# Kernel tuning notes

Measured on AMD Instinct MI355X. Metric: run time of the kernel, lower is better.

Reference implementation:

```python
import jax, jax.numpy as jnp
import numpy as np

L = 2        # gnn_layers
D = 256      # hidden_dim
E = 1024     # emb_dim
NCLS = 7
NEG = 1e30


def lstm_cell(x, h, c, Wih, Whh, bih, bhh):
    # torch.nn.LSTMCell math; gate order i, f, g, o
    g = x @ Wih.T + bih + h @ Whh.T + bhh
    i, f, gg, o = jnp.split(g, 4, axis=-1)
    c2 = jax.nn.sigmoid(f) * c + jax.nn.sigmoid(i) * jnp.tanh(gg)
    return jax.nn.sigmoid(o) * jnp.tanh(c2), c2


def dag_layer(Hl, adj_f, W1, W2, Wr, Wc_ih, Wc_hh, bc_ih, bc_hh, Wp_ih, Wp_hh, bp_ih, bp_hh):
    # Hl: (B,N,D). Sequential DAG recurrence with dot-product attention over growing prefix.
    B, N, Dh = Hl.shape
    zeros = jnp.zeros((B, Dh), Hl.dtype)
    h0 = Hl[:, 0]
    C0, _ = lstm_cell(h0, zeros, zeros, Wc_ih, Wc_hh, bc_ih, bc_hh)
    P0, _ = lstm_cell(zeros, h0, h0, Wp_ih, Wp_hh, bp_ih, bp_hh)
    Ht0 = C0 + P0
    # carry pre-projected keys/values incrementally to avoid O(N^2 D^2) work
    K2 = jnp.zeros((B, N, Dh), Hl.dtype).at[:, 0].set(Ht0 @ W2.T)
    Vr = jnp.zeros((B, N, Dh), Hl.dtype).at[:, 0].set(Ht0 @ Wr.T)
    H1 = jnp.zeros((B, N, Dh), Hl.dtype).at[:, 0].set(Ht0)
    pos = jnp.arange(N)

    def step(carry, i):
        K2, Vr, H1 = carry
        Q = jax.lax.dynamic_index_in_dim(Hl, i, axis=1, keepdims=False)      # (B,D)
        adj_i = jax.lax.dynamic_index_in_dim(adj_f, i, axis=1, keepdims=False)  # (B,N)
        q = Q @ W1.T
        logits = jnp.einsum('bd,bnd->bn', q, K2) - (1.0 - adj_i) * NEG  # mask_logic
        logits = jnp.where(pos[None, :] < i, logits, -NEG)              # only prefix :i
        w = jax.nn.softmax(logits, axis=-1)
        M = jnp.einsum('bn,bnd->bd', w, Vr)
        C, _ = lstm_cell(Q, M, M, Wc_ih, Wc_hh, bc_ih, bc_hh)
        P, _ = lstm_cell(M, Q, Q, Wp_ih, Wp_hh, bp_ih, bp_hh)
        Ht = C + P
        K2 = K2.at[:, i].set(Ht @ W2.T)
        Vr = Vr.at[:, i].set(Ht @ Wr.T)
        H1 = H1.at[:, i].set(Ht)
        return (K2, Vr, H1), None

    (K2, Vr, H1), _ = jax.lax.scan(step, (K2, Vr, H1), jnp.arange(1, N))
    return H1


def setup_inputs() -> dict:
    key = jax.random.key(0)
    ks = iter(jax.random.split(key, 40))
    B, N = 16, 128
    s = lambda *sh: jax.random.normal(next(ks), sh, jnp.float32) * 0.02
    in_dim = D * (L + 1) + E
    return dict(
        features=jax.random.normal(next(ks), (B, N, E), jnp.float32),
        adj=jnp.ones((B, N, N), jnp.int32),
        s_mask=jnp.zeros((B, N, N), jnp.int32),
        s_mask_onehot=jnp.zeros((B, N, N, 2), jnp.int32),
        lengths=jnp.ones((B,), jnp.int32) * N,
        fc1_W=s(D, E), fc1_b=jnp.zeros((D,), jnp.float32),
        W1=s(L, D, D), W2=s(L, D, D), Wr=s(L, D, D),
        Wc_ih=s(L, 4 * D, D), Wc_hh=s(L, 4 * D, D),
        bc_ih=jnp.zeros((L, 4 * D), jnp.float32), bc_hh=jnp.zeros((L, 4 * D), jnp.float32),
        Wp_ih=s(L, 4 * D, D), Wp_hh=s(L, 4 * D, D),
        bp_ih=jnp.zeros((L, 4 * D), jnp.float32), bp_hh=jnp.zeros((L, 4 * D), jnp.float32),
        m0_W=s(D, in_dim), m0_b=jnp.zeros((D,), jnp.float32),
        m1_W=s(D, D), m1_b=jnp.zeros((D,), jnp.float32),
        m2_W=s(NCLS, D), m2_b=jnp.zeros((NCLS,), jnp.float32),
    )


def reference(features, adj, s_mask, s_mask_onehot, lengths,
              fc1_W, fc1_b, W1, W2, Wr,
              Wc_ih, Wc_hh, bc_ih, bc_hh,
              Wp_ih, Wp_hh, bp_ih, bp_hh,
              m0_W, m0_b, m1_W, m1_b, m2_W, m2_b):
    # s_mask / s_mask_onehot unused for attn_type='dotprod', no_rel_attn=True
    # lengths unused for nodal_att_type=None (attentive_node_features is identity)
    adj_f = adj.astype(features.dtype)
    H0 = jax.nn.relu(features @ fc1_W.T + fc1_b)
    Hs = [H0]
    for l in range(L):
        Hs.append(dag_layer(Hs[l], adj_f,
                            W1[l], W2[l], Wr[l],
                            Wc_ih[l], Wc_hh[l], bc_ih[l], bc_hh[l],
                            Wp_ih[l], Wp_hh[l], bp_ih[l], bp_hh[l]))
    Hcat = jnp.concatenate(Hs + [features], axis=2)  # (B,N,D*(L+1)+E)
    h = jax.nn.relu(Hcat @ m0_W.T + m0_b)
    h = jax.nn.relu(h @ m1_W.T + m1_b)  # mlp_layers-1 extra layer; dropout p=0 -> identity
    return h @ m2_W.T + m2_b            # (B,N,num_class)
```

## Files before the change

### kernel.cpp

```cpp
#include <hip/hip_runtime.h>
#include <hip/hip_fp16.h>
#include <math.h>

#define B_ 16
#define N_ 128
#define D_ 256
#define E_ 1024
#define GD4 1024
#define SENT 0xFFC0DEADu

typedef _Float16 h2 __attribute__((ext_vector_type(2)));
typedef _Float16 f16x8 __attribute__((ext_vector_type(8)));
typedef float f32x4 __attribute__((ext_vector_type(4)));

__device__ __forceinline__ float dot2w(unsigned w, h2 hv, float acc) {
#if __has_builtin(__builtin_amdgcn_fdot2)
  return __builtin_amdgcn_fdot2(__builtin_bit_cast(h2, w), hv, acc, false);
#else
  union { unsigned u; _Float16 e[2]; } c; c.u = w;
  return acc + (float)c.e[0]*(float)hv.x + (float)c.e[1]*(float)hv.y;
#endif
}
__device__ __forceinline__ float dot2h(h2 a, h2 b, float acc) {
#if __has_builtin(__builtin_amdgcn_fdot2)
  return __builtin_amdgcn_fdot2(a, b, acc, false);
#else
  return acc + (float)a.x*(float)b.x + (float)a.y*(float)b.y;
#endif
}

template<bool BIAS, bool RELU>
__global__ __launch_bounds__(256) void gemm_k(const float* __restrict__ X,
    const float* __restrict__ W, const float* __restrict__ bias,
    float* __restrict__ C, int M, int N, int K)
{
  __shared__ float Xs[32][68];
  __shared__ float Ws[32][68];
  const int tid = threadIdx.x;
  const int m0 = blockIdx.x * 64, n0 = blockIdx.y * 64;
  const int tm = tid >> 4, tn = tid & 15;
  float acc[4][4] = {};
  for (int k0 = 0; k0 < K; k0 += 32) {
    for (int e = tid; e < 2048; e += 256) {
      int mm = e >> 5, kk = e & 31;
      Xs[kk][mm] = X[(m0+mm)*K + k0+kk];
    }
    for (int e = tid; e < 2048; e += 256) {
      int nn = e >> 5, kk = e & 31;
      Ws[kk][nn] = (n0+nn < N) ? W[(n0+nn)*K + k0+kk] : 0.f;
    }
    __syncthreads();
    for (int kk = 0; kk < 32; kk++) {
      float4 a = *(const float4*)&Xs[kk][tm*4];
      float4 b = *(const float4*)&Ws[kk][tn*4];
      acc[0][0] += a.x*b.x; acc[0][1] += a.x*b.y; acc[0][2] += a.x*b.z; acc[0][3] += a.x*b.w;
      acc[1][0] += a.y*b.x; acc[1][1] += a.y*b.y; acc[1][2] += a.y*b.z; acc[1][3] += a.y*b.w;
      acc[2][0] += a.z*b.x; acc[2][1] += a.z*b.y; acc[2][2] += a.z*b.z; acc[2][3] += a.z*b.w;
      acc[3][0] += a.w*b.x; acc[3][1] += a.w*b.y; acc[3][2] += a.w*b.z; acc[3][3] += a.w*b.w;
    }
    __syncthreads();
  }
  for (int i2 = 0; i2 < 4; i2++) {
    int row = m0 + tm*4 + i2;
    for (int j2 = 0; j2 < 4; j2++) {
      int col = n0 + tn*4 + j2;
      if (col < N) {
        float v = acc[i2][j2];
        if (BIAS) v += bias[col];
        if (RELU) v = fmaxf(v, 0.f);
        C[row*N + col] = v;
      }
    }
  }
}

__device__ __forceinline__ void mf_stage(const float* __restrict__ src,
    int ldsrc, _Float16 (*dst)[264], int tid)
{
  for (int e = tid; e < 8192; e += 256) {
    int row = e >> 7, cp = e & 127;
    float2 v = *(const float2*)&src[(size_t)row*ldsrc + 2*cp];
    h2 t; t.x = (_Float16)v.x; t.y = (_Float16)v.y;
    *(h2*)&dst[row][2*cp] = t;
  }
}

__device__ __forceinline__ void mf_compute(_Float16 (*Xh)[264],
    _Float16 (*Wh)[264], f32x4 acc[2][2], int l, int wr, int wc)
{
  #pragma unroll
  for (int kc = 0; kc < 256; kc += 32) {
    f16x8 a0 = *(const f16x8*)&Xh[wr*32 +      (l & 15)][kc + (l >> 4)*8];
    f16x8 a1 = *(const f16x8*)&Xh[wr*32 + 16 + (l & 15)][kc + (l >> 4)*8];
    f16x8 b0 = *(const f16x8*)&Wh[wc*32 +      (l & 15)][kc + (l >> 4)*8];
    f16x8 b1 = *(const f16x8*)&Wh[wc*32 + 16 + (l & 15)][kc + (l >> 4)*8];
    acc[0][0] = __builtin_amdgcn_mfma_f32_16x16x32_f16(a0, b0, acc[0][0], 0, 0, 0);
    acc[0][1] = __builtin_amdgcn_mfma_f32_16x16x32_f16(a0, b1, acc[0][1], 0, 0, 0);
    acc[1][0] = __builtin_amdgcn_mfma_f32_16x16x32_f16(a1, b0, acc[1][0], 0, 0, 0);
    acc[1][1] = __builtin_amdgcn_mfma_f32_16x16x32_f16(a1, b1, acc[1][1], 0, 0, 0);
  }
}

template<bool BIAS, bool RELU>
__global__ __launch_bounds__(256) void mfgemm_k(const float* __restrict__ X,
    const float* __restrict__ W, const float* __restrict__ bias,
    float* __restrict__ C, int M, int N, int K)
{
  __shared__ _Float16 Xh[64][264];
  __shared__ _Float16 Wh[64][264];
  const int tid = threadIdx.x;
  const int m0 = blockIdx.x * 64, n0 = blockIdx.y * 64;
  const int l = tid & 63, w = tid >> 6;
  const int wr = w >> 1, wc = w & 1;
  f32x4 acc[2][2];
  #pragma unroll
  for (int rt = 0; rt < 2; ++rt)
    #pragma unroll
    for (int ct = 0; ct < 2; ++ct) acc[rt][ct] = 0.f;
  for (int k0 = 0; k0 < K; k0 += 256) {
    mf_stage(X + (size_t)m0*K + k0, K, Xh, tid);
    mf_stage(W + (size_t)n0*K + k0, K, Wh, tid);
    __syncthreads();
    mf_compute(Xh, Wh, acc, l, wr, wc);
    __syncthreads();
  }
  #pragma unroll
  for (int rt = 0; rt < 2; ++rt)
    #pragma unroll
    for (int ct = 0; ct < 2; ++ct)
      #pragma unroll
      for (int j = 0; j < 4; ++j) {
        int row = m0 + wr*32 + rt*16 + (l >> 4)*4 + j;
        int col = n0 + wc*32 + ct*16 + (l & 15);
        float v = acc[rt][ct][j];
        if (BIAS) v += bias[col];
        if (RELU) v = fmaxf(v, 0.f);
        C[(size_t)row*N + col] = v;
      }
}

__global__ __launch_bounds__(256) void prologue_mf_k(const float* __restrict__ X,
    const float* __restrict__ Wc, const float* __restrict__ Wp,
    const float* __restrict__ Am, const float* __restrict__ bcc,
    const float* __restrict__ bpc, float* __restrict__ GQC,
    float* __restrict__ GQP, float* __restrict__ VM)
{
  __shared__ _Float16 Xh[64][264];
  __shared__ _Float16 Wh[64][264];
  const int tid = threadIdx.x;
  const int m0 = blockIdx.x * 64;
  const int nt = blockIdx.y;
  const float* W; const float* bias; float* C; int n0; int NC;
  if (nt < 16)      { W = Wc; bias = bcc;     C = GQC; n0 = nt*64;      NC = 1024; }
  else if (nt < 32) { W = Wp; bias = bpc;     C = GQP; n0 = (nt-16)*64; NC = 1024; }
  else              { W = Am; bias = nullptr; C = VM;  n0 = (nt-32)*64; NC = 256;  }
  const int l = tid & 63, w = tid >> 6;
  const int wr = w >> 1, wc = w & 1;
  f32x4 acc[2][2];
  #pragma unroll
  for (int rt = 0; rt < 2; ++rt)
    #pragma unroll
    for (int ct = 0; ct < 2; ++ct) acc[rt][ct] = 0.f;
  mf_stage(X + (size_t)m0*256, 256, Xh, tid);
  mf_stage(W + (size_t)n0*256, 256, Wh, tid);
  __syncthreads();
  mf_compute(Xh, Wh, acc, l, wr, wc);
  __syncthreads();
  #pragma unroll
  for (int rt = 0; rt < 2; ++rt)
    #pragma unroll
    for (int ct = 0; ct < 2; ++ct)
      #pragma unroll
      for (int j = 0; j < 4; ++j) {
        int row = m0 + wr*32 + rt*16 + (l >> 4)*4 + j;
        int col = n0 + wc*32 + ct*16 + (l & 15);
        float v = acc[rt][ct][j];
        if (bias) v += bias[col];
        C[(size_t)row*NC + col] = v;
      }
}

__global__ __launch_bounds__(256) void m0fused_mf_k(const float* __restrict__ H0,
    const float* __restrict__ H1, const float* __restrict__ H2,
    const float* __restrict__ feat, const float* __restrict__ W,
    const float* __restrict__ bias, float* __restrict__ C)
{
  __shared__ _Float16 Xh[64][264];
  __shared__ _Float16 Wh[64][264];
  const int tid = threadIdx.x;
  const int m0 = blockIdx.x * 64, n0 = blockIdx.y * 64;
  const int l = tid & 63, w = tid >> 6;
  const int wr = w >> 1, wc = w & 1;
  f32x4 acc[2][2];
  #pragma unroll
  for (int rt = 0; rt < 2; ++rt)
    #pragma unroll
    for (int ct = 0; ct < 2; ++ct) acc[rt][ct] = 0.f;
  for (int k0 = 0; k0 < 1792; k0 += 256) {
    const float* src; int lds_; int coff;
    if (k0 == 0)        { src = H0;   lds_ = 256;  coff = 0; }
    else if (k0 == 256) { src = H1;   lds_ = 256;  coff = 0; }
    else if (k0 == 512) { src = H2;   lds_ = 256;  coff = 0; }
    else                { src = feat; lds_ = 1024; coff = k0 - 768; }
    mf_stage(src + (size_t)m0*lds_ + coff, lds_, Xh, tid);
    mf_stage(W + (size_t)n0*1792 + k0, 1792, Wh, tid);
    __syncthreads();
    mf_compute(Xh, Wh, acc, l, wr, wc);
    __syncthreads();
  }
  #pragma unroll
  for (int rt = 0; rt < 2; ++rt)
    #pragma unroll
    for (int ct = 0; ct < 2; ++ct)
      #pragma unroll
      for (int j = 0; j < 4; ++j) {
        int row = m0 + wr*32 + rt*16 + (l >> 4)*4 + j;
        int col = n0 + wc*32 + ct*16 + (l & 15);
        C[(size_t)row*256 + col] = fmaxf(acc[rt][ct][j] + bias[col], 0.f);
      }
}

__global__ __launch_bounds__(256) void prepamat_k(const float* __restrict__ W2,
    const float* __restrict__ W1, float* __restrict__ AM)
{
  __shared__ float Xs[32][68];
  __shared__ float Ws[32][68];
  const int tid = threadIdx.x;
  const int m0 = blockIdx.x * 64, n0 = blockIdx.y * 64;
  const float* X = W2 + blockIdx.z * 65536;
  const float* W = W1 + blockIdx.z * 65536;
  float* C = AM + blockIdx.z * 65536;
  const int tm = tid >> 4, tn = tid & 15;
  float acc[4][4] = {};
  for (int k0 = 0; k0 < 256; k0 += 32) {
    for (int e = tid; e < 2048; e += 256) {
      int kk = e >> 6, mm = e & 63;
      Xs[kk][mm] = X[(k0+kk)*256 + m0+mm];
    }
    for (int e = tid; e < 2048; e += 256) {
      int kk = e >> 6, nn = e & 63;
      Ws[kk][nn] = W[(k0+kk)*256 + n0+nn];
    }
    __syncthreads();
    for (int kk = 0; kk < 32; kk++) {
      float4 a = *(const float4*)&Xs[kk][tm*4];
      float4 b = *(const float4*)&Ws[kk][tn*4];
      acc[0][0] += a.x*b.x; acc[0][1] += a.x*b.y; acc[0][2] += a.x*b.z; acc[0][3] += a.x*b.w;
      acc[1][0] += a.y*b.x; acc[1][1] += a.y*b.y; acc[1][2] += a.y*b.z; acc[1][3] += a.y*b.w;
      acc[2][0] += a.z*b.x; acc[2][1] += a.z*b.y; acc[2][2] += a.z*b.z; acc[2][3] += a.z*b.w;
      acc[3][0] += a.w*b.x; acc[3][1] += a.w*b.y; acc[3][2] += a.w*b.z; acc[3][3] += a.w*b.w;
    }
    __syncthreads();
  }
  for (int i2 = 0; i2 < 4; i2++)
    for (int j2 = 0; j2 < 4; j2++)
      C[(m0 + tm*4 + i2)*256 + n0 + tn*4 + j2] = acc[i2][j2];
}

__global__ __launch_bounds__(256) void prepnn_k(const float* __restrict__ Wch,
    const float* __restrict__ Wpi, const float* __restrict__ Wr,
    float* __restrict__ OUT)
{
  __shared__ float Xs[32][68];
  __shared__ float Ws[32][68];
  const int tid = threadIdx.x;
  const int m0 = blockIdx.x * 64, n0 = blockIdx.y * 64;
  const int l = blockIdx.z;
  const float* X = (m0 < 1024) ? (Wch + l*262144 + m0*256)
                               : (Wpi + l*262144 + (m0-1024)*256);
  const float* W = Wr + l*65536;
  float* C = OUT + l*524288;
  const int tm = tid >> 4, tn = tid & 15;
  float acc[4][4] = {};
  for (int k0 = 0; k0 < 256; k0 += 32) {
    for (int e = tid; e < 2048; e += 256) {
      int mm = e >> 5, kk = e & 31;
      Xs[kk][mm] = X[mm*256 + k0+kk];
    }
    for (int e = tid; e < 2048; e += 256) {
      int kk = e >> 6, nn = e & 63;
      Ws[kk][nn] = W[(k0+kk)*256 + n0+nn];
    }
    __syncthreads();
    for (int kk = 0; kk < 32; kk++) {
      float4 a = *(const float4*)&Xs[kk][tm*4];
      float4 b = *(const float4*)&Ws[kk][tn*4];
      acc[0][0] += a.x*b.x; acc[0][1] += a.x*b.y; acc[0][2] += a.x*b.z; acc[0][3] += a.x*b.w;
      acc[1][0] += a.y*b.x; acc[1][1] += a.y*b.y; acc[1][2] += a.y*b.z; acc[1][3] += a.y*b.w;
      acc[2][0] += a.z*b.x; acc[2][1] += a.z*b.y; acc[2][2] += a.z*b.z; acc[2][3] += a.z*b.w;
      acc[3][0] += a.w*b.x; acc[3][1] += a.w*b.y; acc[3][2] += a.w*b.z; acc[3][3] += a.w*b.w;
    }
    __syncthreads();
  }
  for (int i2 = 0; i2 < 4; i2++)
    for (int j2 = 0; j2 < 4; j2++)
      C[(m0 + tm*4 + i2)*256 + n0 + tn*4 + j2] = acc[i2][j2];
}

__global__ void bias_sum_k(const float* __restrict__ bci, const float* __restrict__ bch,
                           const float* __restrict__ bpi, const float* __restrict__ bph,
                           float* __restrict__ bcC, float* __restrict__ bpC)
{
  int i = blockIdx.x*256 + threadIdx.x;
  if (i < 2048) { bcC[i] = bci[i] + bch[i]; bpC[i] = bpi[i] + bph[i]; }
}

__global__ void pack_k(const float* __restrict__ wchpi, const float* __restrict__ wr,
                       _Float16* __restrict__ out)
{
  int idx = blockIdx.x*256 + threadIdx.x;
  int l  = idx / 589824; int rem = idx % 589824;
  int sl = rem / 36864;  int rem2 = rem % 36864;
  int cq = rem2 / 1152;  int rem3 = rem2 % 1152;
  int r  = rem3 >> 3;    int e = rem3 & 7;
  int c  = cq*8 + e;
  int g  = r >> 4, dl = r & 15;
  int d  = sl*16 + dl;
  float v;
  if (g < 8) v = wchpi[l*524288 + (g*256 + d)*256 + c];
  else       v = wr[l*65536 + d*256 + c];
  out[idx] = (_Float16)v;
}

__global__ void fill_k(unsigned* __restrict__ a, unsigned* __restrict__ b)
{
  int i = blockIdx.x*256 + threadIdx.x;
  if (i < 524288) {
    __hip_atomic_store(a + i, SENT, __ATOMIC_RELAXED, __HIP_MEMORY_SCOPE_AGENT);
    __hip_atomic_store(b + i, SENT, __ATOMIC_RELAXED, __HIP_MEMORY_SCOPE_AGENT);
  }
}

__device__ __forceinline__ float sigf(float x) { return 1.f / (1.f + __expf(-x)); }
__device__ __forceinline__ float tanhfast(float x) {
  float xc = fminf(fmaxf(x, -15.f), 15.f);
  float e = __expf(-2.f * xc);
  return (1.f - e) / (1.f + e);
}

__global__ __launch_bounds__(512, 2) void scan_k(
    const float* __restrict__ Hl,
    const float* __restrict__ Vm,
    const float* __restrict__ gqC,
    const float* __restrict__ gqP,
    const _Float16* __restrict__ WTp,
    const int*   __restrict__ adj,
    float* __restrict__ Hout)
{
  __shared__ uint4 wl4[4608];
  __shared__ float G[128*144];
  __shared__ __align__(8) _Float16 h2s[256];
  __shared__ float v_s[256];
  __shared__ __align__(8) _Float16 v2s[256];
  __shared__ float psum[128];
  __shared__ float aw[128];
  __shared__ int   adj_s[2][128];
  __shared__ float gqc_l[2][64], gqp_l[2][64];
  __shared__ float ql[2][16];
  __shared__ float Gg[144];
  __shared__ float red[2];
  __shared__ float sinv;

  const int tid = threadIdx.x;
  const int b   = blockIdx.x >> 4;
  const int sl  = blockIdx.x & 15;

  { const uint4* src = (const uint4*)WTp + (size_t)sl*4608;
    for (int e = tid; e < 4608; e += 512) wl4[e] = src[e]; }

  const int rr_ = tid >> 2;
  const int rj  = tid & 3;

#define PREF(ip_, bf_) do {                                                    \
    int ip = (ip_); int bf = (bf_);                                            \
    for (int u = tid - 288; u < 528; u += 224) {                               \
      if (u < 256) { float v = Vm[(b*N_ + ip)*D_ + u]; v_s[u] = v;             \
                     v2s[u] = (_Float16)v; }                                   \
      else if (u < 384) adj_s[bf][u-256] = adj[(b*N_ + ip)*N_ + (u-256)];      \
      else if (u < 448) gqc_l[bf][u-384] = gqC[(b*N_+ip)*GD4 + ((u-384)>>4)*D_ + sl*16 + ((u-384)&15)]; \
      else if (u < 512) gqp_l[bf][u-448] = gqP[(b*N_+ip)*GD4 + ((u-448)>>4)*D_ + sl*16 + ((u-448)&15)]; \
      else ql[bf][u-512] = Hl[(b*N_+ip)*D_ + sl*16 + (u-512)];                 \
    }                                                                          \
  } while (0)

  if (tid >= 288) PREF(0, 0);
  __syncthreads();

  for (int i = 0; i < N_; ++i) {
    const int cur = i & 1;
    if (i > 0) {
      if (rr_ + 1 < i) {
        const float4* hp = (const float4*)(Hout + ((size_t)(b*N_ + rr_))*D_) + rj;
        const float4* vv = (const float4*)v_s + rj;
        float4 areg[16];
        #pragma unroll
        for (int c4 = 0; c4 < 16; ++c4) areg[c4] = hp[c4*4];
        float acc = 0.f;
        #pragma unroll
        for (int c4 = 0; c4 < 16; ++c4) {
          float4 a = areg[c4], w = vv[c4*4];
          acc += a.x*w.x + a.y*w.y + a.z*w.z + a.w*w.w;
        }
        acc += __shfl_xor(acc, 1, 64);
        acc += __shfl_xor(acc, 2, 64);
        if (rj == 0) psum[rr_] = acc;
      }
      if (tid >= 448) {
        const unsigned* wp = (const unsigned*)Hout
                           + ((size_t)(b*N_ + (i-1)))*D_ + ((tid-448)&15)*16 + 15;
        while (__hip_atomic_load(wp, __ATOMIC_RELAXED, __HIP_MEMORY_SCOPE_AGENT) == SENT)
          __builtin_amdgcn_s_sleep(1);
        int lane = tid - 448;
        float4 hv = *((const float4*)(Hout + ((size_t)(b*N_ + (i-1)))*D_) + lane);
        h2* hd = (h2*)h2s + lane*2;
        h2 t0; t0.x = (_Float16)hv.x; t0.y = (_Float16)hv.y;
        h2 t1; t1.x = (_Float16)hv.z; t1.y = (_Float16)hv.w;
        hd[0] = t0; hd[1] = t1;
      }
      __syncthreads();
      asm volatile("" ::: "memory");

      if (tid < 288) {
        int r = tid >> 1, hf = tid & 1;
        float acc2 = 0.f;
        #pragma unroll 4
        for (int it = 0; it < 16; ++it) {
          int cq = hf*16 + it;
          uint4 w4 = wl4[cq*144 + r];
          const h2* hh = (const h2*)h2s + cq*4;
          acc2 = dot2w(w4.x, hh[0], acc2);
          acc2 = dot2w(w4.y, hh[1], acc2);
          acc2 = dot2w(w4.z, hh[2], acc2);
          acc2 = dot2w(w4.w, hh[3], acc2);
        }
        acc2 += __shfl_xor(acc2, 1, 64);
        if (!hf) G[(i-1)*144 + r] = acc2;
      }
      if (rr_ == i-1) {
        const h2* hh = (const h2*)h2s + rj*32;
        const h2* vv = (const h2*)v2s + rj*32;
        float acc = 0.f;
        #pragma unroll 8
        for (int q = 0; q < 32; ++q) acc = dot2h(hh[q], vv[q], acc);
        acc += __shfl_xor(acc, 1, 64);
        acc += __shfl_xor(acc, 2, 64);
        if (rj == 0) psum[i-1] = acc;
      }
      if (tid >= 320 && tid < 448) {
        int k = tid - 320;
        float e = (k + 1 < i && adj_s[cur][k] != 0) ? __expf(psum[k]) : 0.f;
        aw[k] = e;
        float sv = e;
        #pragma unroll
        for (int off = 32; off >= 1; off >>= 1) sv += __shfl_xor(sv, off, 64);
        if ((k & 63) == 0) red[k >> 6] = sv;
      }
      __syncthreads();

      if (tid < 288) {
        int r = tid >> 1, kh = tid & 1;
        float e1 = (adj_s[cur][i-1] != 0) ? __expf(psum[i-1]) : 0.f;
        float g = kh ? e1 * G[(i-1)*144 + r] : 0.f;
        int m = i - 1;
        int k0 = kh ? (m >> 1) : 0, k1 = kh ? m : (m >> 1);
        for (int k = k0; k < k1; ++k) g += aw[k] * G[k*144 + r];
        g += __shfl_xor(g, 1, 64);
        if (!kh) Gg[r] = g;
        if (tid == 0) sinv = 1.f / (red[0] + red[1] + e1);
      } else {
        PREF((i < 127) ? i+1 : 127, (i+1) & 1);
      }
      __syncthreads();
    } else {
      if (tid >= 288) PREF(1, 1);
      __syncthreads();
    }

    if (tid < 32) {
      int dl = tid >> 1, cell = tid & 1;
      float inv = (i > 0) ? sinv : 0.f;
      float r0 = 0.f, r1 = 0.f, r2 = 0.f, r3 = 0.f, Mv = 0.f;
      if (i > 0) {
        r0 = Gg[(cell*4+0)*16 + dl] * inv;
        r1 = Gg[(cell*4+1)*16 + dl] * inv;
        r2 = Gg[(cell*4+2)*16 + dl] * inv;
        r3 = Gg[(cell*4+3)*16 + dl] * inv;
        Mv = Gg[128 + dl] * inv;
      }
      float Qv = ql[cur][dl];
      const float* gq = cell ? &gqp_l[cur][0] : &gqc_l[cur][0];
      float xi = cell ? Qv : Mv;
      float gi_ = r0 + gq[ 0 + dl];
      float gf_ = r1 + gq[16 + dl];
      float gg_ = r2 + gq[32 + dl];
      float go_ = r3 + gq[48 + dl];
      float c2  = sigf(gf_)*xi + sigf(gi_)*tanhfast(gg_);
      float ov  = sigf(go_)*tanhfast(c2);
      float htv = ov + __shfl_xor(ov, 1, 64);
      if (!cell) {
        __hip_atomic_store(&Hout[((size_t)(b*N_ + i))*D_ + sl*16 + dl], htv,
                           __ATOMIC_RELAXED, __HIP_MEMORY_SCOPE_AGENT);
      }
    }
  }
#undef PREF
}

extern "C" void kernel_launch(void* const* d_in, const int* in_sizes, int n_in,
                              void* d_out, int out_size, void* d_ws, size_t ws_size,
                              hipStream_t stream)
{
  const float* features = (const float*)d_in[0];
  const int*   adj      = (const int*)  d_in[1];
  const float* fc1_W    = (const float*)d_in[5];
  const float* fc1_b    = (const float*)d_in[6];
  const float* W1       = (const float*)d_in[7];
  const float* W2       = (const float*)d_in[8];
  const float* Wr       = (const float*)d_in[9];
  const float* Wc_ih    = (const float*)d_in[10];
  const float* Wc_hh    = (const float*)d_in[11];
  const float* bc_ih    = (const float*)d_in[12];
  const float* bc_hh    = (const float*)d_in[13];
  const float* Wp_ih    = (const float*)d_in[14];
  const float* Wp_hh    = (const float*)d_in[15];
  const float* bp_ih    = (const float*)d_in[16];
  const float* bp_hh    = (const float*)d_in[17];
  const float* m0_W     = (const float*)d_in[18];
  const float* m0_b     = (const float*)d_in[19];
  const float* m1_W     = (const float*)d_in[20];
  const float* m1_b     = (const float*)d_in[21];
  const float* m2_W     = (const float*)d_in[22];
  const float* m2_b     = (const float*)d_in[23];

  float* ws = (float*)d_ws;
  _Float16* WTP = (_Float16*)ws;
  float* AMAT   = ws + 589824;
  float* BCC    = ws + 720896;
  float* BPC    = ws + 722944;
  float* WCHPI  = ws + 724992;
  float* H0     = ws + 1773568;
  float* H1     = ws + 2297856;
  float* H2     = ws + 2822144;
  float* VMAT   = ws + 3346432;
  float* GQC    = ws + 3870720;
  float* GQP    = ws + 5967872;
  float* HB1    = ws + 8065024;
  float* HB2    = ws + 8589312;

  fill_k<<<2048, 256, 0, stream>>>((unsigned*)H1, (unsigned*)H2);
  bias_sum_k<<<8, 256, 0, stream>>>(bc_ih, bc_hh, bp_ih, bp_hh, BCC, BPC);
  prepamat_k<<<dim3(4,4,2), 256, 0, stream>>>(W2, W1, AMAT);
  prepnn_k<<<dim3(32,4,2), 256, 0, stream>>>(Wc_hh, Wp_ih, Wr, WCHPI);
  pack_k<<<4608, 256, 0, stream>>>(WCHPI, Wr, WTP);

  mfgemm_k<true,true><<<dim3(32,4), 256, 0, stream>>>(features, fc1_W, fc1_b, H0, 2048, 256, 1024);

  prologue_mf_k<<<dim3(32,36), 256, 0, stream>>>(H0, Wc_ih, Wp_hh, AMAT,
                                                 BCC, BPC, GQC, GQP, VMAT);
  scan_k<<<256, 512, 0, stream>>>(H0, VMAT, GQC, GQP, WTP, adj, H1);

  prologue_mf_k<<<dim3(32,36), 256, 0, stream>>>(H1, Wc_ih + 262144, Wp_hh + 262144,
                                                 AMAT + 65536, BCC + 1024, BPC + 1024,
                                                 GQC, GQP, VMAT);
  scan_k<<<256, 512, 0, stream>>>(H1, VMAT, GQC, GQP, WTP + 589824, adj, H2);

  m0fused_mf_k<<<dim3(32,4), 256, 0, stream>>>(H0, H1, H2, features, m0_W, m0_b, HB1);
  mfgemm_k<true,true><<<dim3(32,4), 256, 0, stream>>>(HB1, m1_W, m1_b, HB2, 2048, 256, 256);
  gemm_k<true,false><<<dim3(32,1), 256, 0, stream>>>(HB2, m2_W, m2_b, (float*)d_out, 2048, 7, 256);
}
```

Before: 1.785 ms.

## Fuse weight packing into prep GEMM, drop bias kernel, shrink sentinel fill

Measured after the change: 1.824 ms. 2.2% more time.

```diff
diff --git a/kernel.cpp b/kernel.cpp
--- a/kernel.cpp
+++ b/kernel.cpp
@@ -141,8 +141,9 @@
 
 __global__ __launch_bounds__(256) void prologue_mf_k(const float* __restrict__ X,
     const float* __restrict__ Wc, const float* __restrict__ Wp,
-    const float* __restrict__ Am, const float* __restrict__ bcc,
-    const float* __restrict__ bpc, float* __restrict__ GQC,
+    const float* __restrict__ Am, const float* __restrict__ bci,
+    const float* __restrict__ bch, const float* __restrict__ bpi,
+    const float* __restrict__ bph, float* __restrict__ GQC,
     float* __restrict__ GQP, float* __restrict__ VM)
 {
   __shared__ _Float16 Xh[64][264];
@@ -150,10 +151,10 @@
   const int tid = threadIdx.x;
   const int m0 = blockIdx.x * 64;
   const int nt = blockIdx.y;
-  const float* W; const float* bias; float* C; int n0; int NC;
-  if (nt < 16)      { W = Wc; bias = bcc;     C = GQC; n0 = nt*64;      NC = 1024; }
-  else if (nt < 32) { W = Wp; bias = bpc;     C = GQP; n0 = (nt-16)*64; NC = 1024; }
-  else              { W = Am; bias = nullptr; C = VM;  n0 = (nt-32)*64; NC = 256;  }
+  const float* W; const float* b0; const float* b1; float* C; int n0; int NC;
+  if (nt < 16)      { W = Wc; b0 = bci; b1 = bch;  C = GQC; n0 = nt*64;      NC = 1024; }
+  else if (nt < 32) { W = Wp; b0 = bpi; b1 = bph;  C = GQP; n0 = (nt-16)*64; NC = 1024; }
+  else              { W = Am; b0 = nullptr; b1 = nullptr; C = VM; n0 = (nt-32)*64; NC = 256; }
   const int l = tid & 63, w = tid >> 6;
   const int wr = w >> 1, wc = w & 1;
   f32x4 acc[2][2];
@@ -175,7 +176,7 @@
         int row = m0 + wr*32 + rt*16 + (l >> 4)*4 + j;
         int col = n0 + wc*32 + ct*16 + (l & 15);
         float v = acc[rt][ct][j];
-        if (bias) v += bias[col];
+        if (b0) v += b0[col] + b1[col];
         C[(size_t)row*NC + col] = v;
       }
 }
@@ -259,7 +260,7 @@
 
 __global__ __launch_bounds__(256) void prepnn_k(const float* __restrict__ Wch,
     const float* __restrict__ Wpi, const float* __restrict__ Wr,
-    float* __restrict__ OUT)
+    _Float16* __restrict__ WTP)
 {
   __shared__ float Xs[32][68];
   __shared__ float Ws[32][68];
@@ -269,7 +270,6 @@
   const float* X = (m0 < 1024) ? (Wch + l*262144 + m0*256)
                                : (Wpi + l*262144 + (m0-1024)*256);
   const float* W = Wr + l*65536;
-  float* C = OUT + l*524288;
   const int tm = tid >> 4, tn = tid & 15;
   float acc[4][4] = {};
   for (int k0 = 0; k0 < 256; k0 += 32) {
@@ -292,42 +292,35 @@
     }
     __syncthreads();
   }
-  for (int i2 = 0; i2 < 4; i2++)
-    for (int j2 = 0; j2 < 4; j2++)
-      C[(m0 + tm*4 + i2)*256 + n0 + tn*4 + j2] = acc[i2][j2];
-}
-
-__global__ void bias_sum_k(const float* __restrict__ bci, const float* __restrict__ bch,
-                           const float* __restrict__ bpi, const float* __restrict__ bph,
-                           float* __restrict__ bcC, float* __restrict__ bpC)
+  for (int i2 = 0; i2 < 4; i2++) {
+    int row = m0 + tm*4 + i2;
+    int g = (row < 1024) ? (row >> 8) : (4 + ((row - 1024) >> 8));
+    int d = row & 255;
+    int slp = d >> 4, dl = d & 15, r = g*16 + dl;
+    size_t base = (size_t)l*589824 + (size_t)slp*36864 + r*8;
+    for (int j2 = 0; j2 < 4; j2++) {
+      int c = n0 + tn*4 + j2;
+      WTP[base + (size_t)(c >> 3)*1152 + (c & 7)] = (_Float16)acc[i2][j2];
+    }
+  }
+}
+
+__global__ void wrpack_k(const float* __restrict__ wr, _Float16* __restrict__ WTP)
+{
+  int idx = blockIdx.x*256 + threadIdx.x;
+  int l = idx >> 16; int rem = idx & 65535;
+  int d = rem >> 8; int c = rem & 255;
+  int slp = d >> 4, dl = d & 15;
+  WTP[(size_t)l*589824 + (size_t)slp*36864 + (size_t)(c >> 3)*1152
+      + (128 + dl)*8 + (c & 7)] = (_Float16)wr[l*65536 + d*256 + c];
+}
+
+__global__ void fill_k(unsigned* __restrict__ a, unsigned* __restrict__ b)
 {
   int i = blockIdx.x*256 + threadIdx.x;
-  if (i < 2048) { bcC[i] = bci[i] + bch[i]; bpC[i] = bpi[i] + bph[i]; }
-}
-
-__global__ void pack_k(const float* __restrict__ wchpi, const float* __restrict__ wr,
-                       _Float16* __restrict__ out)
-{
-  int idx = blockIdx.x*256 + threadIdx.x;
-  int l  = idx / 589824; int rem = idx % 589824;
-  int sl = rem / 36864;  int rem2 = rem % 36864;
-  int cq = rem2 / 1152;  int rem3 = rem2 % 1152;
-  int r  = rem3 >> 3;    int e = rem3 & 7;
-  int c  = cq*8 + e;
-  int g  = r >> 4, dl = r & 15;
-  int d  = sl*16 + dl;
-  float v;
-  if (g < 8) v = wchpi[l*524288 + (g*256 + d)*256 + c];
-  else       v = wr[l*65536 + d*256 + c];
-  out[idx] = (_Float16)v;
-}
-
-__global__ void fill_k(unsigned* __restrict__ a, unsigned* __restrict__ b)
-{
-  int i = blockIdx.x*256 + threadIdx.x;
-  if (i < 524288) {
-    __hip_atomic_store(a + i, SENT, __ATOMIC_RELAXED, __HIP_MEMORY_SCOPE_AGENT);
-    __hip_atomic_store(b + i, SENT, __ATOMIC_RELAXED, __HIP_MEMORY_SCOPE_AGENT);
+  if (i < 32768) {
+    __hip_atomic_store(a + i*16 + 15, SENT, __ATOMIC_RELAXED, __HIP_MEMORY_SCOPE_AGENT);
+    __hip_atomic_store(b + i*16 + 15, SENT, __ATOMIC_RELAXED, __HIP_MEMORY_SCOPE_AGENT);
   }
 }
 
@@ -406,13 +399,16 @@
         if (rj == 0) psum[rr_] = acc;
       }
       if (tid >= 448) {
+        int L = tid - 448;
         const unsigned* wp = (const unsigned*)Hout
-                           + ((size_t)(b*N_ + (i-1)))*D_ + ((tid-448)&15)*16 + 15;
-        while (__hip_atomic_load(wp, __ATOMIC_RELAXED, __HIP_MEMORY_SCOPE_AGENT) == SENT)
-          __builtin_amdgcn_s_sleep(1);
-        int lane = tid - 448;
-        float4 hv = *((const float4*)(Hout + ((size_t)(b*N_ + (i-1)))*D_) + lane);
-        h2* hd = (h2*)h2s + lane*2;
+                           + ((size_t)(b*N_ + (i-1)))*D_ + (L & 15)*16 + 15;
+        unsigned v;
+        do {
+          v = (L < 16) ? __hip_atomic_load(wp, __ATOMIC_RELAXED, __HIP_MEMORY_SCOPE_AGENT)
+                       : 0u;
+        } while (__ballot((L < 16) && (v == SENT)));
+        float4 hv = *((const float4*)(Hout + ((size_t)(b*N_ + (i-1)))*D_) + L);
+        h2* hd = (h2*)h2s + L*2;
         h2 t0; t0.x = (_Float16)hv.x; t0.y = (_Float16)hv.y;
         h2 t1; t1.x = (_Float16)hv.z; t1.y = (_Float16)hv.w;
         hd[0] = t0; hd[1] = t1;
@@ -535,32 +531,31 @@
   float* ws = (float*)d_ws;
   _Float16* WTP = (_Float16*)ws;
   float* AMAT   = ws + 589824;
-  float* BCC    = ws + 720896;
-  float* BPC    = ws + 722944;
-  float* WCHPI  = ws + 724992;
-  float* H0     = ws + 1773568;
-  float* H1     = ws + 2297856;
-  float* H2     = ws + 2822144;
-  float* VMAT   = ws + 3346432;
-  float* GQC    = ws + 3870720;
-  float* GQP    = ws + 5967872;
-  float* HB1    = ws + 8065024;
-  float* HB2    = ws + 8589312;
-
-  fill_k<<<2048, 256, 0, stream>>>((unsigned*)H1, (unsigned*)H2);
-  bias_sum_k<<<8, 256, 0, stream>>>(bc_ih, bc_hh, bp_ih, bp_hh, BCC, BPC);
+  float* H0     = ws + 720896;
+  float* H1     = ws + 1245184;
+  float* H2     = ws + 1769472;
+  float* VMAT   = ws + 2293760;
+  float* GQC    = ws + 2818048;
+  float* GQP    = ws + 4915200;
+  float* HB1    = ws + 7012352;
+  float* HB2    = ws + 7536640;
+
+  fill_k<<<128, 256, 0, stream>>>((unsigned*)H1, (unsigned*)H2);
   prepamat_k<<<dim3(4,4,2), 256, 0, stream>>>(W2, W1, AMAT);
-  prepnn_k<<<dim3(32,4,2), 256, 0, stream>>>(Wc_hh, Wp_ih, Wr, WCHPI);
-  pack_k<<<4608, 256, 0, stream>>>(WCHPI, Wr, WTP);
+  prepnn_k<<<dim3(32,4,2), 256, 0, stream>>>(Wc_hh, Wp_ih, Wr, WTP);
+  wrpack_k<<<512, 256, 0, stream>>>(Wr, WTP);
 
   mfgemm_k<true,true><<<dim3(32,4), 256, 0, stream>>>(features, fc1_W, fc1_b, H0, 2048, 256, 1024);
 
   prologue_mf_k<<<dim3(32,36), 256, 0, stream>>>(H0, Wc_ih, Wp_hh, AMAT,
-                                                 BCC, BPC, GQC, GQP, VMAT);
+                                                 bc_ih, bc_hh, bp_ih, bp_hh,
+                                                 GQC, GQP, VMAT);
   scan_k<<<256, 512, 0, stream>>>(H0, VMAT, GQC, GQP, WTP, adj, H1);
 
   prologue_mf_k<<<dim3(32,36), 256, 0, stream>>>(H1, Wc_ih + 262144, Wp_hh + 262144,
-                                                 AMAT + 65536, BCC + 1024, BPC + 1024,
+                                                 AMAT + 65536,
+                                                 bc_ih + 1024, bc_hh + 1024,
+                                                 bp_ih + 1024, bp_hh + 1024,
                                                  GQC, GQP, VMAT);
   scan_k<<<256, 512, 0, stream>>>(H1, VMAT, GQC, GQP, WTP + 589824, adj, H2);
 
```
